# Performance work log

Measured on AMD Instinct MI355X. Metric: run time of the kernel, lower is better.

Reference implementation:

```python
import jax, jax.numpy as jnp
import numpy as np

V, D, L, H, FF, S = 32000, 400, 6, 8, 1600, 2048
B, N = 2, 2048
HD = D // H


def setup_inputs() -> dict:
    key = jax.random.key(0)
    ks = jax.random.split(key, 9)
    n = lambda k, shape: 0.02 * jax.random.normal(k, shape, dtype=jnp.float32)
    return {
        "idx": jax.random.randint(ks[0], (B, N), 0, V),
        "tok_emb": n(ks[1], (V, D)),
        "pos_emb": n(ks[2], (S, D)),
        "ln1_w": jnp.ones((L, D), jnp.float32), "ln1_b": jnp.zeros((L, D), jnp.float32),
        "qkv_w": n(ks[3], (L, D, 3 * D)), "qkv_b": jnp.zeros((L, 3 * D), jnp.float32),
        "attn_out_w": n(ks[4], (L, D, D)), "attn_out_b": jnp.zeros((L, D), jnp.float32),
        "ln2_w": jnp.ones((L, D), jnp.float32), "ln2_b": jnp.zeros((L, D), jnp.float32),
        "fc1_w": n(ks[5], (L, D, FF)), "fc1_b": jnp.zeros((L, FF), jnp.float32),
        "fc2_w": n(ks[6], (L, FF, D)), "fc2_b": jnp.zeros((L, D), jnp.float32),
        "lnf_w": jnp.ones((D,), jnp.float32), "lnf_b": jnp.zeros((D,), jnp.float32),
        "head_w": n(ks[7], (D, V)),
    }


def _ln(x, w, b):
    m = x.mean(-1, keepdims=True)
    v = ((x - m) ** 2).mean(-1, keepdims=True)
    return (x - m) * jax.lax.rsqrt(v + 1e-5) * w + b


def reference(idx, tok_emb, pos_emb, ln1_w, ln1_b, qkv_w, qkv_b, attn_out_w, attn_out_b,
              ln2_w, ln2_b, fc1_w, fc1_b, fc2_w, fc2_b, lnf_w, lnf_b, head_w):
    b, n = idx.shape
    scale = HD ** -0.5
    x = tok_emb[idx] + pos_emb[None, :n]          # [B,N,D]
    mask = jnp.tril(jnp.ones((n, n), dtype=bool))  # causal mask
    for l in range(L):
        h = _ln(x, ln1_w[l], ln1_b[l])
        qkv = h @ qkv_w[l] + qkv_b[l]
        q, k, v = jnp.split(qkv, 3, axis=-1)
        q = q.reshape(b, n, H, HD)
        k = k.reshape(b, n, H, HD)
        v = v.reshape(b, n, H, HD)
        s = jnp.einsum('bihd,bjhd->bhij', q, k) * scale   # [B,H,N,N]
        s = jnp.where(mask, s, -jnp.inf)
        a = jax.nn.softmax(s, axis=-1)
        o = jnp.einsum('bhij,bjhd->bihd', a, v).reshape(b, n, D)
        x = x + o @ attn_out_w[l] + attn_out_b[l]
        h = _ln(x, ln2_w[l], ln2_b[l])
        x = x + jax.nn.gelu(h @ fc1_w[l] + fc1_b[l], approximate=False) @ fc2_w[l] + fc2_b[l]
    return _ln(x, lnf_w, lnf_b) @ head_w          # [B,N,V] logits
```

## Files before the change

### kernel.cpp

```cpp
#include <hip/hip_runtime.h>
#include <hip/hip_bf16.h>
#include <math.h>

constexpr int V  = 32000;
constexpr int D  = 400;
constexpr int L  = 6;
constexpr int H  = 8;
constexpr int FF = 1600;
constexpr int B  = 2;
constexpr int N  = 2048;
constexpr int HD = D / H;
constexpr int TD = 3 * D;
constexpr int M  = B * N;
constexpr int KP = 416;

typedef __bf16 bf16x8 __attribute__((ext_vector_type(8)));
typedef float  f32x4  __attribute__((ext_vector_type(4)));
typedef unsigned short us16x4 __attribute__((ext_vector_type(4)));

static __device__ __forceinline__ float wave_sum_f(float v) {
#pragma unroll
    for (int m = 32; m; m >>= 1) v += __shfl_xor(v, m, 64);
    return v;
}

static __device__ __forceinline__ void gl_lds16(const unsigned short* g, unsigned short* l) {
    __builtin_amdgcn_global_load_lds(
        (const __attribute__((address_space(1))) unsigned int*)(g),
        (__attribute__((address_space(3))) unsigned int*)(l), 16, 0, 0);
}

static __device__ __forceinline__ unsigned short f2bf(float f) {
    __hip_bfloat16 h = __float2bfloat16(f);
    return *reinterpret_cast<unsigned short*>(&h);
}

__global__ __launch_bounds__(256) void embed_kernel(const int* __restrict__ idx,
                                                    const float* __restrict__ tok,
                                                    const float* __restrict__ pos,
                                                    float* __restrict__ x) {
    size_t i = (size_t)blockIdx.x * 256 + threadIdx.x;
    if (i >= (size_t)M * D) return;
    int d  = (int)(i % D);
    int bn = (int)(i / D);
    int n  = bn % N;
    x[i] = tok[(size_t)idx[bn] * D + d] + pos[(size_t)n * D + d];
}

__global__ __launch_bounds__(256) void wconv_kernel(const float* __restrict__ W,
                                                    __hip_bfloat16* __restrict__ Bt,
                                                    int K, int Nw, int Kp, int Nr,
                                                    long sW, long sBt) {
    const int l = blockIdx.z;
    __shared__ float t[32][33];
    const int k0 = blockIdx.x * 32, n0 = blockIdx.y * 32;
    const float* Wl = W + (size_t)l * sW;
    __hip_bfloat16* Btl = Bt + (size_t)l * sBt;
    for (int i = 0; i < 32; i += 8) {
        int k = k0 + threadIdx.y + i, n = n0 + threadIdx.x;
        t[threadIdx.y + i][threadIdx.x] = (k < K && n < Nw) ? Wl[(size_t)k * Nw + n] : 0.f;
    }
    __syncthreads();
    for (int i = 0; i < 32; i += 8) {
        int n = n0 + threadIdx.y + i, k = k0 + threadIdx.x;
        if (n < Nr && k < Kp) Btl[(size_t)n * Kp + k] = __float2bfloat16(t[threadIdx.x][threadIdx.y + i]);
    }
}

__global__ __launch_bounds__(256) void ln_bf16_kernel(const float* __restrict__ in,
                                                      const float* __restrict__ w,
                                                      const float* __restrict__ b,
                                                      __hip_bfloat16* __restrict__ out) {
    const int row  = blockIdx.x * 4 + (threadIdx.x >> 6);
    const int lane = threadIdx.x & 63;
    const float* xr = in + (size_t)row * D;
    float s = 0.f, ss = 0.f;
    for (int d = lane; d < D; d += 64) {
        float v = xr[d];
        s += v; ss += v * v;
    }
    s  = wave_sum_f(s);
    ss = wave_sum_f(ss);
    float mean = s * (1.0f / D);
    float var  = ss * (1.0f / D) - mean * mean;
    float rstd = rsqrtf(var + 1e-5f);
    __hip_bfloat16* orow = out + (size_t)row * KP;
    for (int d = lane; d < KP; d += 64)
        orow[d] = __float2bfloat16(d < D ? (xr[d] - mean) * rstd * w[d] + b[d] : 0.f);
}

template <bool BIAS, bool RES, bool GELU, bool OUTBF>
__global__ __launch_bounds__(256) void mm_kernel(const unsigned short* __restrict__ A,
                                                 const unsigned short* __restrict__ Bt,
                                                 const float* __restrict__ bias,
                                                 const float* __restrict__ res,
                                                 void* __restrict__ Cv,
                                                 int Nc, int Kp) {
    __shared__ __align__(1024) unsigned short As[128 * 32];
    __shared__ __align__(1024) unsigned short Bs[128 * 32];
    const int tid  = threadIdx.x;
    const int lane = tid & 63, wid = tid >> 6;
    const int wr = wid >> 1, wc = wid & 1;
    const int bx = blockIdx.x, by = blockIdx.y;

    f32x4 acc[4][4] = {};

    const unsigned short* Abase = A  + (size_t)(by * 128) * Kp;
    const unsigned short* Bbase = Bt + (size_t)(bx * 128) * Kp;
    const int lrow = lane >> 2;
    const int lcol = (lane & 3) * 8;

    for (int k0 = 0; k0 < Kp; k0 += 32) {
#pragma unroll
        for (int c = 0; c < 2; ++c) {
            const int chunk = wid * 2 + c;
            gl_lds16(Abase + (size_t)(chunk * 16 + lrow) * Kp + k0 + lcol, As + chunk * 512);
            gl_lds16(Bbase + (size_t)(chunk * 16 + lrow) * Kp + k0 + lcol, Bs + chunk * 512);
        }
        __syncthreads();
        bf16x8 a[4], b[4];
#pragma unroll
        for (int m = 0; m < 4; ++m)
            a[m] = *(const bf16x8*)(As + (wr * 64 + m * 16 + (lane & 15)) * 32 + (lane >> 4) * 8);
#pragma unroll
        for (int n = 0; n < 4; ++n)
            b[n] = *(const bf16x8*)(Bs + (wc * 64 + n * 16 + (lane & 15)) * 32 + (lane >> 4) * 8);
#pragma unroll
        for (int m = 0; m < 4; ++m)
#pragma unroll
            for (int n = 0; n < 4; ++n)
                acc[m][n] = __builtin_amdgcn_mfma_f32_16x16x32_bf16(a[m], b[n], acc[m][n], 0, 0, 0);
        __syncthreads();
    }

    const int col_base = bx * 128 + wc * 64 + (lane & 15);
    const int row_base = by * 128 + wr * 64 + ((lane >> 4) << 2);
#pragma unroll
    for (int n = 0; n < 4; ++n) {
        const int col = col_base + n * 16;
        if (col >= Nc) continue;
        const float bv = BIAS ? bias[col] : 0.f;
#pragma unroll
        for (int m = 0; m < 4; ++m) {
#pragma unroll
            for (int r = 0; r < 4; ++r) {
                const int row = row_base + m * 16 + r;
                float v = acc[m][n][r] + bv;
                if (GELU) v = 0.5f * v * (1.0f + erff(v * 0.70710678118654752f));
                const size_t ci = (size_t)row * Nc + col;
                if (RES) v += res[ci];
                if (OUTBF) ((__hip_bfloat16*)Cv)[ci] = __float2bfloat16(v);
                else       ((float*)Cv)[ci] = v;
            }
        }
    }
}

template <bool BIAS, bool RES, bool GELU, bool OUTBF>
__global__ __launch_bounds__(256) void mm64_kernel(const unsigned short* __restrict__ A,
                                                   const unsigned short* __restrict__ Bt,
                                                   const float* __restrict__ bias,
                                                   const float* __restrict__ res,
                                                   void* __restrict__ Cv,
                                                   int Nc, int Kp) {
    __shared__ __align__(1024) unsigned short As[64 * 32];
    __shared__ __align__(1024) unsigned short Bs[128 * 32];
    const int tid  = threadIdx.x;
    const int lane = tid & 63, wid = tid >> 6;
    const int wr = wid >> 1, wc = wid & 1;
    const int bx = blockIdx.x, by = blockIdx.y;
    const int l15 = lane & 15, g = lane >> 4;

    f32x4 acc[2][4] = {};

    const unsigned short* Abase = A  + (size_t)(by * 64) * Kp;
    const unsigned short* Bbase = Bt + (size_t)(bx * 128) * Kp;
    const int lrow = lane >> 2;
    const int lcol = (lane & 3) * 8;

    for (int k0 = 0; k0 < Kp; k0 += 32) {
        gl_lds16(Abase + (size_t)(wid * 16 + lrow) * Kp + k0 + lcol, As + wid * 512);
#pragma unroll
        for (int c = 0; c < 2; ++c) {
            const int chunk = wid * 2 + c;
            gl_lds16(Bbase + (size_t)(chunk * 16 + lrow) * Kp + k0 + lcol, Bs + chunk * 512);
        }
        __syncthreads();
        bf16x8 a[2], b[4];
#pragma unroll
        for (int m = 0; m < 2; ++m)
            a[m] = *(const bf16x8*)(As + (wr * 32 + m * 16 + l15) * 32 + g * 8);
#pragma unroll
        for (int n = 0; n < 4; ++n)
            b[n] = *(const bf16x8*)(Bs + (wc * 64 + n * 16 + l15) * 32 + g * 8);
#pragma unroll
        for (int m = 0; m < 2; ++m)
#pragma unroll
            for (int n = 0; n < 4; ++n)
                acc[m][n] = __builtin_amdgcn_mfma_f32_16x16x32_bf16(a[m], b[n], acc[m][n], 0, 0, 0);
        __syncthreads();
    }

    const int col_base = bx * 128 + wc * 64 + l15;
    const int row_base = by * 64 + wr * 32 + (g << 2);
#pragma unroll
    for (int n = 0; n < 4; ++n) {
        const int col = col_base + n * 16;
        if (col >= Nc) continue;
        const float bv = BIAS ? bias[col] : 0.f;
#pragma unroll
        for (int m = 0; m < 2; ++m) {
#pragma unroll
            for (int r = 0; r < 4; ++r) {
                const int row = row_base + m * 16 + r;
                float v = acc[m][n][r] + bv;
                if (GELU) v = 0.5f * v * (1.0f + erff(v * 0.70710678118654752f));
                const size_t ci = (size_t)row * Nc + col;
                if (RES) v += res[ci];
                if (OUTBF) ((__hip_bfloat16*)Cv)[ci] = __float2bfloat16(v);
                else       ((float*)Cv)[ci] = v;
            }
        }
    }
}

__global__ __launch_bounds__(256) void mm_qkv_kernel(const unsigned short* __restrict__ A,
                                                     const unsigned short* __restrict__ Bt,
                                                     const float* __restrict__ bias,
                                                     unsigned short* __restrict__ Qb,
                                                     unsigned short* __restrict__ Kb,
                                                     unsigned short* __restrict__ Vt) {
    __shared__ __align__(1024) unsigned short As[128 * 32];
    __shared__ __align__(1024) unsigned short Bs[128 * 32];
    const int tid  = threadIdx.x;
    const int lane = tid & 63, wid = tid >> 6;
    const int wr = wid >> 1, wc = wid & 1;
    const int bx = blockIdx.x, by = blockIdx.y;

    f32x4 acc[4][4] = {};

    const unsigned short* Abase = A  + (size_t)(by * 128) * KP;
    const unsigned short* Bbase = Bt + (size_t)(bx * 128) * KP;
    const int lrow = lane >> 2;
    const int lcol = (lane & 3) * 8;

    for (int k0 = 0; k0 < KP; k0 += 32) {
#pragma unroll
        for (int c = 0; c < 2; ++c) {
            const int chunk = wid * 2 + c;
            gl_lds16(Abase + (size_t)(chunk * 16 + lrow) * KP + k0 + lcol, As + chunk * 512);
            gl_lds16(Bbase + (size_t)(chunk * 16 + lrow) * KP + k0 + lcol, Bs + chunk * 512);
        }
        __syncthreads();
        bf16x8 a[4], b[4];
#pragma unroll
        for (int m = 0; m < 4; ++m)
            a[m] = *(const bf16x8*)(As + (wr * 64 + m * 16 + (lane & 15)) * 32 + (lane >> 4) * 8);
#pragma unroll
        for (int n = 0; n < 4; ++n)
            b[n] = *(const bf16x8*)(Bs + (wc * 64 + n * 16 + (lane & 15)) * 32 + (lane >> 4) * 8);
#pragma unroll
        for (int m = 0; m < 4; ++m)
#pragma unroll
            for (int n = 0; n < 4; ++n)
                acc[m][n] = __builtin_amdgcn_mfma_f32_16x16x32_bf16(a[m], b[n], acc[m][n], 0, 0, 0);
        __syncthreads();
    }

    const float scale = 0.14142135623730950f;
    const int col_base = bx * 128 + wc * 64 + (lane & 15);
    const int row_base = by * 128 + wr * 64 + ((lane >> 4) << 2);
#pragma unroll
    for (int n = 0; n < 4; ++n) {
        const int col = col_base + n * 16;
        if (col >= TD) continue;
        const int part = col < D ? 0 : (col < 2 * D ? 1 : 2);
        const int cc = col - part * D;
        const int h = cc / HD, d = cc % HD;
        const float bv = bias[col];
#pragma unroll
        for (int m = 0; m < 4; ++m) {
            const int row0 = row_base + m * 16;
            const int b = row0 >> 11, nn0 = row0 & (N - 1);
            const int bh = b * H + h;
            if (part == 2) {
                us16x4 pk;
#pragma unroll
                for (int r = 0; r < 4; ++r) pk[r] = f2bf(acc[m][n][r] + bv);
                *(us16x4*)(Vt + (size_t)(bh * 64 + d) * N + nn0) = pk;
            } else if (part == 0) {
#pragma unroll
                for (int r = 0; r < 4; ++r)
                    Qb[(size_t)(bh * N + nn0 + r) * 64 + d] = f2bf((acc[m][n][r] + bv) * scale);
            } else {
#pragma unroll
                for (int r = 0; r < 4; ++r)
                    Kb[(size_t)(bh * N + nn0 + r) * 64 + d] = f2bf(acc[m][n][r] + bv);
            }
        }
    }
}

__global__ __launch_bounds__(256) void fattn_kernel(const unsigned short* __restrict__ Qb,
                                                    const unsigned short* __restrict__ Kb,
                                                    const unsigned short* __restrict__ Vt,
                                                    __hip_bfloat16* __restrict__ o) {
    const int q0 = blockIdx.x * 64, h = blockIdx.y, b = blockIdx.z;
    const int bh = b * H + h;
    const int tid = threadIdx.x, lane = tid & 63, w = tid >> 6;
    const int l15 = lane & 15, g = lane >> 4;

    __shared__ __align__(1024) unsigned short Ks[2][64 * 64];
    __shared__ __align__(1024) unsigned short Vs[2][64 * 64];
    __shared__ __hip_bfloat16 P_s[4][16 * 72];
    unsigned short* Pw = (unsigned short*)&P_s[w][0];

    const int st_r    = (lane >> 3);
    const int st_cblk = (lane ^ (lane >> 3)) & 7;

    const unsigned short* Qrow = Qb + ((size_t)(bh * N + q0 + w * 16 + l15)) * 64 + g * 8;
    const bf16x8 qa0 = *(const bf16x8*)(Qrow);
    const bf16x8 qa1 = *(const bf16x8*)(Qrow + 32);

    f32x4 acc[4] = {};
    float ssum[4] = {0.f, 0.f, 0.f, 0.f};

    const int nt = q0 / 64 + 1;

#define STAGE(buf, j0)                                                                     \
    {                                                                                      \
        _Pragma("unroll")                                                                  \
        for (int c = 0; c < 2; ++c) {                                                      \
            const int rr = (w * 2 + c) * 8 + st_r;                                         \
            gl_lds16(Kb + (size_t)(bh * N + (j0) + rr) * 64 + st_cblk * 8,                 \
                     &Ks[buf][(w * 2 + c) * 512]);                                         \
            gl_lds16(Vt + (size_t)(bh * 64 + rr) * N + (j0) + st_cblk * 8,                 \
                     &Vs[buf][(w * 2 + c) * 512]);                                         \
        }                                                                                  \
    }

    STAGE(0, 0);
    __syncthreads();

    for (int t = 0; t < nt; ++t) {
        const int cur = t & 1;
        if (t + 1 < nt) STAGE(cur ^ 1, (t + 1) * 64);

        f32x4 s[4];
        const int swz = ((l15 & 7) << 3);
#pragma unroll
        for (int n = 0; n < 4; ++n) {
            const unsigned short* kbase = &Ks[cur][(n * 16 + l15) * 64];
            bf16x8 k0 = *(const bf16x8*)(kbase + ((g * 8) ^ swz));
            bf16x8 k1 = *(const bf16x8*)(kbase + (((g + 4) * 8) ^ swz));
            f32x4 z = {};
            z    = __builtin_amdgcn_mfma_f32_16x16x32_bf16(qa0, k0, z, 0, 0, 0);
            s[n] = __builtin_amdgcn_mfma_f32_16x16x32_bf16(qa1, k1, z, 0, 0, 0);
        }
        if (t == nt - 1) {
#pragma unroll
            for (int n = 0; n < 4; ++n)
#pragma unroll
                for (int r = 0; r < 4; ++r)
                    if (l15 + n * 16 > w * 16 + g * 4 + r) s[n][r] = -INFINITY;
        }
#pragma unroll
        for (int n = 0; n < 4; ++n)
#pragma unroll
            for (int r = 0; r < 4; ++r) {
                float p = __expf(s[n][r]);
                ssum[r] += p;
                Pw[(g * 4 + r) * 72 + l15 + n * 16] = f2bf(p);
            }
        bf16x8 pa0 = *(const bf16x8*)(Pw + l15 * 72 + g * 8);
        bf16x8 pa1 = *(const bf16x8*)(Pw + l15 * 72 + 32 + g * 8);

#pragma unroll
        for (int n = 0; n < 4; ++n) {
            const unsigned short* vbase = &Vs[cur][(n * 16 + l15) * 64];
            bf16x8 v0 = *(const bf16x8*)(vbase + ((g * 8) ^ swz));
            bf16x8 v1 = *(const bf16x8*)(vbase + (((g + 4) * 8) ^ swz));
            acc[n] = __builtin_amdgcn_mfma_f32_16x16x32_bf16(pa0, v0, acc[n], 0, 0, 0);
            acc[n] = __builtin_amdgcn_mfma_f32_16x16x32_bf16(pa1, v1, acc[n], 0, 0, 0);
        }

        __syncthreads();
    }
#undef STAGE

#pragma unroll
    for (int r = 0; r < 4; ++r)
#pragma unroll
        for (int msk = 1; msk < 16; msk <<= 1) ssum[r] += __shfl_xor(ssum[r], msk, 64);

#pragma unroll
    for (int n = 0; n < 4; ++n) {
        const int d = n * 16 + l15;
        if (d < HD) {
#pragma unroll
            for (int r = 0; r < 4; ++r) {
                const int row = b * N + q0 + w * 16 + g * 4 + r;
                o[(size_t)row * KP + h * HD + d] = __float2bfloat16(acc[n][r] / ssum[r]);
            }
        }
    }
}

extern "C" void kernel_launch(void* const* d_in, const int* in_sizes, int n_in,
                              void* d_out, int out_size, void* d_ws, size_t ws_size,
                              hipStream_t stream) {
    const int*   idx        = (const int*)d_in[0];
    const float* tok_emb    = (const float*)d_in[1];
    const float* pos_emb    = (const float*)d_in[2];
    const float* ln1_w      = (const float*)d_in[3];
    const float* ln1_b      = (const float*)d_in[4];
    const float* qkv_w      = (const float*)d_in[5];
    const float* qkv_b      = (const float*)d_in[6];
    const float* attn_out_w = (const float*)d_in[7];
    const float* attn_out_b = (const float*)d_in[8];
    const float* ln2_w      = (const float*)d_in[9];
    const float* ln2_b      = (const float*)d_in[10];
    const float* fc1_w      = (const float*)d_in[11];
    const float* fc1_b      = (const float*)d_in[12];
    const float* fc2_w      = (const float*)d_in[13];
    const float* fc2_b      = (const float*)d_in[14];
    const float* lnf_w      = (const float*)d_in[15];
    const float* lnf_b      = (const float*)d_in[16];
    const float* head_w     = (const float*)d_in[17];
    float* out = (float*)d_out;

    char* ws = (char*)d_ws;
    __hip_bfloat16* hb   = (__hip_bfloat16*)(ws);
    float*          x    = (float*)(ws + 3407872);
    __hip_bfloat16* ff   = (__hip_bfloat16*)(ws + 9961472);
    __hip_bfloat16* ob   = (__hip_bfloat16*)(ws + 23068672);
    __hip_bfloat16* headt = (__hip_bfloat16*)(ws + 3407872);

    char* wout = (char*)d_out;
    __hip_bfloat16* qkvt = (__hip_bfloat16*)(wout);
    __hip_bfloat16* aot  = (__hip_bfloat16*)(wout + 6389760);
    __hip_bfloat16* fc1t = (__hip_bfloat16*)(wout + 8945664);
    __hip_bfloat16* fc2t = (__hip_bfloat16*)(wout + 17252352);
    unsigned short* qb_g = (unsigned short*)(wout + 27082752);
    unsigned short* kb_g = (unsigned short*)(wout + 31277056);
    unsigned short* vt_g = (unsigned short*)(wout + 35471360);

    const dim3 tb(32, 8);
    wconv_kernel<<<dim3(13, 40, L), tb, 0, stream>>>(qkv_w,      qkvt, D,  TD, KP, 1280, (long)D * TD, 1280L * KP);
    wconv_kernel<<<dim3(13, 16, L), tb, 0, stream>>>(attn_out_w, aot,  D,  D,  KP, 512,  (long)D * D,  512L * KP);
    wconv_kernel<<<dim3(13, 52, L), tb, 0, stream>>>(fc1_w,      fc1t, D,  FF, KP, 1664, (long)D * FF, 1664L * KP);
    wconv_kernel<<<dim3(50, 16, L), tb, 0, stream>>>(fc2_w,      fc2t, FF, D,  FF, 512,  (long)FF * D, 512L * (long)FF);

    embed_kernel<<<dim3((M * D + 255) / 256), dim3(256), 0, stream>>>(idx, tok_emb, pos_emb, x);
    hipMemsetAsync(ob, 0, (size_t)M * KP * sizeof(__hip_bfloat16), stream);
    hipMemsetAsync(qb_g, 0, 3 * 4194304, stream);

    for (int l = 0; l < L; ++l) {
        ln_bf16_kernel<<<dim3(M / 4), dim3(256), 0, stream>>>(x, ln1_w + (size_t)l * D, ln1_b + (size_t)l * D, hb);
        mm_qkv_kernel<<<dim3(10, 32), dim3(256), 0, stream>>>(
            (const unsigned short*)hb, (const unsigned short*)(qkvt + (size_t)l * 1280 * KP),
            qkv_b + (size_t)l * TD, qb_g, kb_g, vt_g);
        fattn_kernel<<<dim3(N / 64, H, B), dim3(256), 0, stream>>>(qb_g, kb_g, vt_g, ob);
        mm64_kernel<true, true, false, false><<<dim3(4, 64), dim3(256), 0, stream>>>(
            (const unsigned short*)ob, (const unsigned short*)(aot + (size_t)l * 512 * KP),
            attn_out_b + (size_t)l * D, x, x, D, KP);
        ln_bf16_kernel<<<dim3(M / 4), dim3(256), 0, stream>>>(x, ln2_w + (size_t)l * D, ln2_b + (size_t)l * D, hb);
        mm_kernel<true, false, true, true><<<dim3(13, 32), dim3(256), 0, stream>>>(
            (const unsigned short*)hb, (const unsigned short*)(fc1t + (size_t)l * 1664 * KP),
            fc1_b + (size_t)l * FF, nullptr, ff, FF, KP);
        mm64_kernel<true, true, false, false><<<dim3(4, 64), dim3(256), 0, stream>>>(
            (const unsigned short*)ff, (const unsigned short*)(fc2t + (size_t)l * 512 * FF),
            fc2_b + (size_t)l * D, x, x, D, FF);
    }

    ln_bf16_kernel<<<dim3(M / 4), dim3(256), 0, stream>>>(x, lnf_w, lnf_b, hb);
    wconv_kernel<<<dim3(13, 1000, 1), tb, 0, stream>>>(head_w, headt, D, V, KP, V, 0, 0);
    mm_kernel<false, false, false, false><<<dim3(V / 128, 32), dim3(256), 0, stream>>>(
        (const unsigned short*)hb, (const unsigned short*)headt, nullptr, nullptr, out, V, KP);
}
```

Baseline: 1.169 ms.

## Merge weight conversions, fuse embed with first LN, swizzle head GEMM blocks

Folds the four per-matrix weight transpose/convert launches into one flat-grid kernel, and fuses the embedding gather with the first layer norm. The per-layer LN1 is moved to the end of the previous iteration, and the final LN is merged into the last iteration. The head GEMM grid is remapped so consecutive blocks in each XCD group share B tiles, aiming for better L2 reuse. Together these cut launch count and one full pass over x, at the cost of hardcoded tile tables that must match the shapes.

```diff
diff --git a/kernel.cpp b/kernel.cpp
--- a/kernel.cpp
+++ b/kernel.cpp
@@ -35,35 +35,46 @@
     return *reinterpret_cast<unsigned short*>(&h);
 }
 
-__global__ __launch_bounds__(256) void embed_kernel(const int* __restrict__ idx,
-                                                    const float* __restrict__ tok,
-                                                    const float* __restrict__ pos,
-                                                    float* __restrict__ x) {
-    size_t i = (size_t)blockIdx.x * 256 + threadIdx.x;
-    if (i >= (size_t)M * D) return;
-    int d  = (int)(i % D);
-    int bn = (int)(i / D);
-    int n  = bn % N;
-    x[i] = tok[(size_t)idx[bn] * D + d] + pos[(size_t)n * D + d];
-}
-
-__global__ __launch_bounds__(256) void wconv_kernel(const float* __restrict__ W,
-                                                    __hip_bfloat16* __restrict__ Bt,
-                                                    int K, int Nw, int Kp, int Nr,
-                                                    long sW, long sBt) {
-    const int l = blockIdx.z;
-    __shared__ float t[32][33];
-    const int k0 = blockIdx.x * 32, n0 = blockIdx.y * 32;
-    const float* Wl = W + (size_t)l * sW;
-    __hip_bfloat16* Btl = Bt + (size_t)l * sBt;
-    for (int i = 0; i < 32; i += 8) {
-        int k = k0 + threadIdx.y + i, n = n0 + threadIdx.x;
-        t[threadIdx.y + i][threadIdx.x] = (k < K && n < Nw) ? Wl[(size_t)k * Nw + n] : 0.f;
-    }
-    __syncthreads();
-    for (int i = 0; i < 32; i += 8) {
-        int n = n0 + threadIdx.y + i, k = k0 + threadIdx.x;
-        if (n < Nr && k < Kp) Btl[(size_t)n * Kp + k] = __float2bfloat16(t[threadIdx.x][threadIdx.y + i]);
+__global__ __launch_bounds__(256) void embed_ln_kernel(const int* __restrict__ idx,
+                                                       const float* __restrict__ tok,
+                                                       const float* __restrict__ pos,
+                                                       const float* __restrict__ lnw,
+                                                       const float* __restrict__ lnb,
+                                                       float* __restrict__ x,
+                                                       __hip_bfloat16* __restrict__ hb) {
+    const int row  = blockIdx.x * 4 + (threadIdx.x >> 6);
+    const int lane = threadIdx.x & 63;
+    const int n = row & (N - 1);
+    const float* tr = tok + (size_t)idx[row] * D;
+    const float* pr = pos + (size_t)n * D;
+
+    float v[7];
+    float s = 0.f, ss = 0.f;
+#pragma unroll
+    for (int i = 0; i < 7; ++i) {
+        const int d = lane + i * 64;
+        if (d < D) {
+            v[i] = tr[d] + pr[d];
+            s += v[i]; ss += v[i] * v[i];
+        } else v[i] = 0.f;
+    }
+    s  = wave_sum_f(s);
+    ss = wave_sum_f(ss);
+    const float mean = s * (1.0f / D);
+    const float var  = ss * (1.0f / D) - mean * mean;
+    const float rstd = rsqrtf(var + 1e-5f);
+
+    float* xr = x + (size_t)row * D;
+    __hip_bfloat16* hr = hb + (size_t)row * KP;
+#pragma unroll
+    for (int i = 0; i < 7; ++i) {
+        const int d = lane + i * 64;
+        if (d < D) {
+            xr[d] = v[i];
+            hr[d] = __float2bfloat16((v[i] - mean) * rstd * lnw[d] + lnb[d]);
+        } else if (d < KP) {
+            hr[d] = __float2bfloat16(0.f);
+        }
     }
 }
 
@@ -89,7 +100,66 @@
         orow[d] = __float2bfloat16(d < D ? (xr[d] - mean) * rstd * w[d] + b[d] : 0.f);
 }
 
-template <bool BIAS, bool RES, bool GELU, bool OUTBF>
+__global__ __launch_bounds__(256) void wconv_all_kernel(const float* __restrict__ qkv_w,
+                                                        const float* __restrict__ ao_w,
+                                                        const float* __restrict__ fc1_w,
+                                                        const float* __restrict__ fc2_w,
+                                                        __hip_bfloat16* __restrict__ qkvt,
+                                                        __hip_bfloat16* __restrict__ aot,
+                                                        __hip_bfloat16* __restrict__ fc1t,
+                                                        __hip_bfloat16* __restrict__ fc2t) {
+    const int bid = blockIdx.x;
+    int t, rem;
+    if      (bid < 3120) { t = 0; rem = bid; }
+    else if (bid < 4368) { t = 1; rem = bid - 3120; }
+    else if (bid < 8424) { t = 2; rem = bid - 4368; }
+    else                 { t = 3; rem = bid - 8424; }
+    const int  tilesPerL[4] = {520, 208, 676, 800};
+    const int  nkt[4]  = {13, 13, 13, 50};
+    const int  Ka[4]   = {400, 400, 400, 1600};
+    const int  Nwa[4]  = {1200, 400, 1600, 400};
+    const int  Kpa[4]  = {416, 416, 416, 1600};
+    const int  Nra[4]  = {1280, 512, 1664, 512};
+    const long sWa[4]  = {480000L, 160000L, 640000L, 640000L};
+    const long sBta[4] = {532480L, 212992L, 692224L, 819200L};
+    const float* W = t == 0 ? qkv_w : t == 1 ? ao_w : t == 2 ? fc1_w : fc2_w;
+    __hip_bfloat16* Bt = t == 0 ? qkvt : t == 1 ? aot : t == 2 ? fc1t : fc2t;
+    const int l = rem / tilesPerL[t];
+    const int tile = rem % tilesPerL[t];
+    const int k0 = (tile % nkt[t]) * 32, n0 = (tile / nkt[t]) * 32;
+    const int K = Ka[t], Nw = Nwa[t], Kp = Kpa[t], Nr = Nra[t];
+
+    __shared__ float tt[32][33];
+    const float* Wl = W + (size_t)l * sWa[t];
+    __hip_bfloat16* Btl = Bt + (size_t)l * sBta[t];
+    for (int i = 0; i < 32; i += 8) {
+        int k = k0 + threadIdx.y + i, n = n0 + threadIdx.x;
+        tt[threadIdx.y + i][threadIdx.x] = (k < K && n < Nw) ? Wl[(size_t)k * Nw + n] : 0.f;
+    }
+    __syncthreads();
+    for (int i = 0; i < 32; i += 8) {
+        int n = n0 + threadIdx.y + i, k = k0 + threadIdx.x;
+        if (n < Nr && k < Kp) Btl[(size_t)n * Kp + k] = __float2bfloat16(tt[threadIdx.x][threadIdx.y + i]);
+    }
+}
+
+__global__ __launch_bounds__(256) void wconv_kernel(const float* __restrict__ W,
+                                                    __hip_bfloat16* __restrict__ Bt,
+                                                    int K, int Nw, int Kp, int Nr) {
+    __shared__ float t[32][33];
+    const int k0 = blockIdx.x * 32, n0 = blockIdx.y * 32;
+    for (int i = 0; i < 32; i += 8) {
+        int k = k0 + threadIdx.y + i, n = n0 + threadIdx.x;
+        t[threadIdx.y + i][threadIdx.x] = (k < K && n < Nw) ? W[(size_t)k * Nw + n] : 0.f;
+    }
+    __syncthreads();
+    for (int i = 0; i < 32; i += 8) {
+        int n = n0 + threadIdx.y + i, k = k0 + threadIdx.x;
+        if (n < Nr && k < Kp) Bt[(size_t)n * Kp + k] = __float2bfloat16(t[threadIdx.x][threadIdx.y + i]);
+    }
+}
+
+template <bool BIAS, bool RES, bool GELU, bool OUTBF, bool XCDSWZ = false>
 __global__ __launch_bounds__(256) void mm_kernel(const unsigned short* __restrict__ A,
                                                  const unsigned short* __restrict__ Bt,
                                                  const float* __restrict__ bias,
@@ -101,7 +171,15 @@
     const int tid  = threadIdx.x;
     const int lane = tid & 63, wid = tid >> 6;
     const int wr = wid >> 1, wc = wid & 1;
-    const int bx = blockIdx.x, by = blockIdx.y;
+    int bx, by;
+    if (XCDSWZ) {
+        const int f   = blockIdx.y * gridDim.x + blockIdx.x;
+        const int swz = (f & 7) * 1000 + (f >> 3);
+        by = swz & 31;
+        bx = swz >> 5;
+    } else {
+        bx = blockIdx.x; by = blockIdx.y;
+    }
 
     f32x4 acc[4][4] = {};
 
@@ -445,18 +523,14 @@
     unsigned short* kb_g = (unsigned short*)(wout + 31277056);
     unsigned short* vt_g = (unsigned short*)(wout + 35471360);
 
-    const dim3 tb(32, 8);
-    wconv_kernel<<<dim3(13, 40, L), tb, 0, stream>>>(qkv_w,      qkvt, D,  TD, KP, 1280, (long)D * TD, 1280L * KP);
-    wconv_kernel<<<dim3(13, 16, L), tb, 0, stream>>>(attn_out_w, aot,  D,  D,  KP, 512,  (long)D * D,  512L * KP);
-    wconv_kernel<<<dim3(13, 52, L), tb, 0, stream>>>(fc1_w,      fc1t, D,  FF, KP, 1664, (long)D * FF, 1664L * KP);
-    wconv_kernel<<<dim3(50, 16, L), tb, 0, stream>>>(fc2_w,      fc2t, FF, D,  FF, 512,  (long)FF * D, 512L * (long)FF);
-
-    embed_kernel<<<dim3((M * D + 255) / 256), dim3(256), 0, stream>>>(idx, tok_emb, pos_emb, x);
+    wconv_all_kernel<<<dim3(13224), dim3(32, 8), 0, stream>>>(
+        qkv_w, attn_out_w, fc1_w, fc2_w, qkvt, aot, fc1t, fc2t);
+
+    embed_ln_kernel<<<dim3(M / 4), dim3(256), 0, stream>>>(idx, tok_emb, pos_emb, ln1_w, ln1_b, x, hb);
     hipMemsetAsync(ob, 0, (size_t)M * KP * sizeof(__hip_bfloat16), stream);
     hipMemsetAsync(qb_g, 0, 3 * 4194304, stream);
 
     for (int l = 0; l < L; ++l) {
-        ln_bf16_kernel<<<dim3(M / 4), dim3(256), 0, stream>>>(x, ln1_w + (size_t)l * D, ln1_b + (size_t)l * D, hb);
         mm_qkv_kernel<<<dim3(10, 32), dim3(256), 0, stream>>>(
             (const unsigned short*)hb, (const unsigned short*)(qkvt + (size_t)l * 1280 * KP),
             qkv_b + (size_t)l * TD, qb_g, kb_g, vt_g);
@@ -471,10 +545,12 @@
         mm64_kernel<true, true, false, false><<<dim3(4, 64), dim3(256), 0, stream>>>(
             (const unsigned short*)ff, (const unsigned short*)(fc2t + (size_t)l * 512 * FF),
             fc2_b + (size_t)l * D, x, x, D, FF);
-    }
-
-    ln_bf16_kernel<<<dim3(M / 4), dim3(256), 0, stream>>>(x, lnf_w, lnf_b, hb);
-    wconv_kernel<<<dim3(13, 1000, 1), tb, 0, stream>>>(head_w, headt, D, V, KP, V, 0, 0);
-    mm_kernel<false, false, false, false><<<dim3(V / 128, 32), dim3(256), 0, stream>>>(
+        const float* nw = (l < L - 1) ? ln1_w + (size_t)(l + 1) * D : lnf_w;
+        const float* nb = (l < L - 1) ? ln1_b + (size_t)(l + 1) * D : lnf_b;
+        ln_bf16_kernel<<<dim3(M / 4), dim3(256), 0, stream>>>(x, nw, nb, hb);
+    }
+
+    wconv_kernel<<<dim3(13, 1000), dim3(32, 8), 0, stream>>>(head_w, headt, D, V, KP, V);
+    mm_kernel<false, false, false, false, true><<<dim3(32, 250), dim3(256), 0, stream>>>(
         (const unsigned short*)hb, (const unsigned short*)headt, nullptr, nullptr, out, V, KP);
 }
```

Measured after the change: 1.163 ms. About the same (-0.5%).
